# Performance work log

Hardware: AMD Instinct MI355X
Metric: run time of the kernel (lower is better)

Reference implementation:

```python
import jax, jax.numpy as jnp
import numpy as np

B, E, R, A, NV, SEL = 512, 1024, 1024, 512, 196, 36

def _lstm_cell(x, h, c, Wih, bih, Whh, bhh):
    g = x @ Wih.T + bih + h @ Whh.T + bhh
    i, f, gg, o = jnp.split(g, 4, axis=1)  # torch gate order i,f,g,o
    c2 = jax.nn.sigmoid(f) * c + jax.nn.sigmoid(i) * jnp.tanh(gg)
    h2 = jax.nn.sigmoid(o) * jnp.tanh(c2)
    return h2, c2

def _attention(h, feats, p_feats, Wh, bh, Wa, ba):
    # feats: [B,S,R], p_feats: [B,S,A]
    att_h = h @ Wh.T + bh                       # [B,A]
    dot = jnp.tanh(p_feats + att_h[:, None, :])  # [B,S,A]
    scores = jnp.einsum('bsa,a->bs', dot, Wa[0]) + ba[0]
    w = jax.nn.softmax(scores, axis=1)
    return jnp.einsum('bs,bsd->bd', w, feats)

def setup_inputs() -> dict:
    key = jax.random.key(0)
    ks = jax.random.split(key, 32)
    s = 0.02
    inp = {
        'xt': jax.random.normal(ks[0], (B, E), jnp.float32),
        'fc_feats': jax.random.normal(ks[1], (B, R), jnp.float32),
        'att_feats': jax.random.normal(ks[2], (B, NV, R), jnp.float32),
        'p_att_feats': jax.random.normal(ks[3], (B, NV, A), jnp.float32),
        'state_h': jax.random.normal(ks[4], (2, B, R), jnp.float32),
        'state_c': jax.random.normal(ks[5], (2, B, R), jnp.float32),
        # att_lstm: input E + 2R
        'W_ih_att': jax.random.normal(ks[6], (4 * R, E + 2 * R), jnp.float32) * s,
        'b_ih_att': jnp.zeros((4 * R,), jnp.float32),
        'W_hh_att': jax.random.normal(ks[7], (4 * R, R), jnp.float32) * s,
        'b_hh_att': jnp.zeros((4 * R,), jnp.float32),
        # lang_lstm: input 3R
        'W_ih_lang': jax.random.normal(ks[8], (4 * R, 3 * R), jnp.float32) * s,
        'b_ih_lang': jnp.zeros((4 * R,), jnp.float32),
        'W_hh_lang': jax.random.normal(ks[9], (4 * R, R), jnp.float32) * s,
        'b_hh_lang': jnp.zeros((4 * R,), jnp.float32),
        # attention 1
        'Wh2att1': jax.random.normal(ks[10], (A, R), jnp.float32) * s,
        'bh2att1': jnp.zeros((A,), jnp.float32),
        'Walpha1': jax.random.normal(ks[11], (1, A), jnp.float32) * s,
        'balpha1': jnp.zeros((1,), jnp.float32),
        # vf attention
        'Wh2att2': jax.random.normal(ks[12], (A, R), jnp.float32) * s,
        'bh2att2': jnp.zeros((A,), jnp.float32),
        'Walpha2': jax.random.normal(ks[13], (1, A), jnp.float32) * s,
        'balpha2': jnp.zeros((1,), jnp.float32),
        # vf_layer and p_vf
        'W_vf': jax.random.normal(ks[14], (NV, 2 * R), jnp.float32) * s,
        'b_vf': jnp.zeros((NV,), jnp.float32),
        'W_pvf': jax.random.normal(ks[15], (A, R), jnp.float32) * s,
        'b_pvf': jnp.zeros((A,), jnp.float32),
    }
    return inp

def reference(xt, fc_feats, att_feats, p_att_feats, state_h, state_c,
              W_ih_att, b_ih_att, W_hh_att, b_hh_att,
              W_ih_lang, b_ih_lang, W_hh_lang, b_hh_lang,
              Wh2att1, bh2att1, Walpha1, balpha1,
              Wh2att2, bh2att2, Walpha2, balpha2,
              W_vf, b_vf, W_pvf, b_pvf):
    # dropout in eval mode -> identity
    prev_h = state_h[-1]
    att_lstm_input = jnp.concatenate([prev_h, fc_feats, xt], axis=1)
    h_att, c_att = _lstm_cell(att_lstm_input, state_h[0], state_c[0],
                              W_ih_att, b_ih_att, W_hh_att, b_hh_att)
    att = _attention(h_att, att_feats, p_att_feats, Wh2att1, bh2att1, Walpha1, balpha1)
    conc = jnp.concatenate([att, h_att], axis=1)          # [B,2R]
    vf_ha = conc @ W_vf.T + b_vf                          # [B,NV]
    vf_soft = jax.nn.softmax(vf_ha, axis=1)
    _, vf_ix = jax.lax.top_k(vf_soft, SEL)                # [B,SEL] (descending)
    arr1 = jnp.take_along_axis(att_feats, vf_ix[:, :, None], axis=1)  # [B,SEL,R]
    p_vf_feats = arr1 @ W_pvf.T + b_pvf                   # [B,SEL,A]
    vf_att = _attention(h_att, arr1, p_vf_feats, Wh2att2, bh2att2, Walpha2, balpha2)
    lang_lstm_input = jnp.concatenate([vf_att, h_att, att], axis=1)
    h_lang, c_lang = _lstm_cell(lang_lstm_input, state_h[1], state_c[1],
                                W_ih_lang, b_ih_lang, W_hh_lang, b_hh_lang)
    output = h_lang
    new_h = jnp.stack([h_att, h_lang])
    new_c = jnp.stack([c_att, c_lang])
    return output, new_h, new_c
```

## Files before the change

kernel.cpp:

```cpp
#include <hip/hip_runtime.h>

typedef __attribute__((ext_vector_type(4))) float f32x4;
typedef __attribute__((ext_vector_type(8))) _Float16 half8;
typedef __attribute__((ext_vector_type(4))) _Float16 half4;

__device__ __forceinline__ float fast_tanh(float x) {
  float e = __expf(2.f * x);
  return 1.f - 2.f / (e + 1.f);
}
__device__ __forceinline__ float fast_sigmoid(float x) {
  return 1.f / (1.f + __expf(-x));
}

__device__ __forceinline__ void gl_lds16(const _Float16* g, _Float16* l) {
  __builtin_amdgcn_global_load_lds(
      (const __attribute__((address_space(1))) void*)g,
      (__attribute__((address_space(3))) void*)l, 16, 0, 0);
}

template<int SPLIT, int OUT16, int NGUARD, int SWAPXY>
__global__ __launch_bounds__(256) void gemm16(
    const _Float16* __restrict__ Ahp, const _Float16* __restrict__ Alp, int lda,
    const _Float16* __restrict__ Bhp, const _Float16* __restrict__ Blp, int ldb,
    void* __restrict__ Cp, int ldc, long czstride,
    int N, int Kc)
{
  __shared__ _Float16 sAh[2][128 * 32];
  __shared__ _Float16 sBh[2][128 * 32];
  __shared__ _Float16 sAl[SPLIT == 3 ? 2 : 1][SPLIT == 3 ? 128 * 32 : 8];
  __shared__ _Float16 sBl[SPLIT == 3 ? 2 : 1][SPLIT == 3 ? 128 * 32 : 8];

  const int tid = threadIdx.x, lane = tid & 63, wid = tid >> 6;
  const int wm = wid >> 1, wn = wid & 1;
  const int l16 = lane & 15, k8 = lane >> 4;
  const int sr = lane >> 2;
  const int scol = ((lane & 3) ^ ((lane >> 3) & 3)) * 8;
  const int koff = ((k8 ^ ((lane >> 1) & 3))) * 8;

  const int  kt0   = blockIdx.z * Kc;
  const long abase = (long)(SWAPXY ? blockIdx.x : blockIdx.y) * 128;
  const long bbase = (long)(SWAPXY ? blockIdx.y : blockIdx.x) * 128;

  const int r0 = wid * 32 + sr;
  const int r1 = wid * 32 + 16 + sr;
  long br0 = bbase + r0, br1 = bbase + r1;
  if (NGUARD) {
    if (br0 > N - 1) br0 = N - 1;
    if (br1 > N - 1) br1 = N - 1;
  }

  const _Float16* ga0 = Ahp + (abase + r0) * (long)lda + kt0 + scol;
  const _Float16* ga1 = Ahp + (abase + r1) * (long)lda + kt0 + scol;
  const _Float16* gb0 = Bhp + br0 * (long)ldb + kt0 + scol;
  const _Float16* gb1 = Bhp + br1 * (long)ldb + kt0 + scol;
  const _Float16* la0 = SPLIT == 3 ? Alp + (abase + r0) * (long)lda + kt0 + scol : nullptr;
  const _Float16* la1 = SPLIT == 3 ? Alp + (abase + r1) * (long)lda + kt0 + scol : nullptr;
  const _Float16* lb0 = SPLIT == 3 ? Blp + br0 * (long)ldb + kt0 + scol : nullptr;
  const _Float16* lb1 = SPLIT == 3 ? Blp + br1 * (long)ldb + kt0 + scol : nullptr;

  const int e0 = (wid * 32) * 32;
  const int e1 = (wid * 32 + 16) * 32;

  f32x4 acc[4][4];
#pragma unroll
  for (int i = 0; i < 4; i++)
#pragma unroll
    for (int j = 0; j < 4; j++) acc[i][j] = (f32x4){0.f, 0.f, 0.f, 0.f};

  auto STAGE = [&](int buf, int kk) {
    gl_lds16(ga0 + kk, &sAh[buf][e0]);
    gl_lds16(ga1 + kk, &sAh[buf][e1]);
    gl_lds16(gb0 + kk, &sBh[buf][e0]);
    gl_lds16(gb1 + kk, &sBh[buf][e1]);
    if (SPLIT == 3) {
      gl_lds16(la0 + kk, &sAl[buf][e0]);
      gl_lds16(la1 + kk, &sAl[buf][e1]);
      gl_lds16(lb0 + kk, &sBl[buf][e0]);
      gl_lds16(lb1 + kk, &sBl[buf][e1]);
    }
  };

  STAGE(0, 0);

  const int nst = Kc >> 5;
  for (int t = 0; t < nst; t++) {
    const int buf = t & 1;
    if (t + 1 < nst) {
      STAGE(buf ^ 1, (t + 1) * 32);
      if (SPLIT == 3) asm volatile("s_waitcnt vmcnt(8)" ::: "memory");
      else            asm volatile("s_waitcnt vmcnt(4)" ::: "memory");
    } else {
      asm volatile("s_waitcnt vmcnt(0)" ::: "memory");
    }
    __builtin_amdgcn_sched_barrier(0);
    __builtin_amdgcn_s_barrier();
    __builtin_amdgcn_sched_barrier(0);

    half8 ah[4], bh[4];
#pragma unroll
    for (int m = 0; m < 4; m++)
      ah[m] = *(const half8*)&sAh[buf][(wm * 64 + m * 16 + l16) * 32 + koff];
#pragma unroll
    for (int n = 0; n < 4; n++)
      bh[n] = *(const half8*)&sBh[buf][(wn * 64 + n * 16 + l16) * 32 + koff];
#pragma unroll
    for (int m = 0; m < 4; m++)
#pragma unroll
      for (int n = 0; n < 4; n++)
        acc[m][n] = __builtin_amdgcn_mfma_f32_16x16x32_f16(ah[m], bh[n], acc[m][n], 0, 0, 0);
    if (SPLIT == 3) {
      half8 al[4], bl[4];
#pragma unroll
      for (int m = 0; m < 4; m++)
        al[m] = *(const half8*)&sAl[buf][(wm * 64 + m * 16 + l16) * 32 + koff];
#pragma unroll
      for (int n = 0; n < 4; n++)
        bl[n] = *(const half8*)&sBl[buf][(wn * 64 + n * 16 + l16) * 32 + koff];
#pragma unroll
      for (int m = 0; m < 4; m++)
#pragma unroll
        for (int n = 0; n < 4; n++) {
          acc[m][n] = __builtin_amdgcn_mfma_f32_16x16x32_f16(al[m], bh[n], acc[m][n], 0, 0, 0);
          acc[m][n] = __builtin_amdgcn_mfma_f32_16x16x32_f16(ah[m], bl[n], acc[m][n], 0, 0, 0);
        }
    }
    __builtin_amdgcn_sched_barrier(0);
    __builtin_amdgcn_s_barrier();
    __builtin_amdgcn_sched_barrier(0);
  }

  const long czoff = (long)blockIdx.z * czstride;
#pragma unroll
  for (int m = 0; m < 4; m++)
#pragma unroll
    for (int n = 0; n < 4; n++) {
      const long row0 = abase + wm * 64 + m * 16 + (lane >> 4) * 4;
      const long col  = bbase + wn * 64 + n * 16 + l16;
      if (!NGUARD || col < N) {
#pragma unroll
        for (int j = 0; j < 4; j++) {
          const long idx = (row0 + j) * (long)ldc + col + czoff;
          if (OUT16) ((_Float16*)Cp)[idx] = (_Float16)acc[m][n][j];
          else       ((float*)Cp)[idx] = acc[m][n][j];
        }
      }
    }
}

__global__ __launch_bounds__(256) void pack_kernel(
    const float* __restrict__ xt, const float* __restrict__ fc,
    const float* __restrict__ sh,
    _Float16* __restrict__ X1h, _Float16* __restrict__ X1l)
{
  int i = blockIdx.x * 256 + threadIdx.x;
  int b = i >> 10, rr = i & 1023;
  long base = (long)b * 4096;
  float v[4];
  v[0] = sh[524288 + i];
  v[1] = fc[i];
  v[2] = xt[i];
  v[3] = sh[i];
#pragma unroll
  for (int j = 0; j < 4; j++) {
    _Float16 h = (_Float16)v[j];
    X1h[base + j * 1024 + rr] = h;
    X1l[base + j * 1024 + rr] = (_Float16)(v[j] - (float)h);
  }
}

__global__ __launch_bounds__(256) void convertA_kernel(
    const float* __restrict__ WihA, const float* __restrict__ WhhA,
    const float* __restrict__ Wh1, const float* __restrict__ Wh2,
    const float* __restrict__ Wvf, const float* __restrict__ Wpvf,
    _Float16* __restrict__ WcAh, _Float16* __restrict__ WcAl,
    _Float16* __restrict__ W12h, _Float16* __restrict__ Wvfh,
    _Float16* __restrict__ Wvfl, _Float16* __restrict__ Wpvfh)
{
  int bi = blockIdx.x, t = threadIdx.x;
  if (bi < 16384) {
    long e = ((long)bi * 256 + t) * 4;
    int row = (int)(e >> 12), col = (int)(e & 4095);
    const float* src = (col < 3072) ? WihA + (long)row * 3072 + col
                                    : WhhA + (long)row * 1024 + (col - 3072);
    f32x4 v = *(const f32x4*)src;
    half4 h, l;
#pragma unroll
    for (int j = 0; j < 4; j++) { h[j] = (_Float16)v[j]; l[j] = (_Float16)(v[j] - (float)h[j]); }
    *(half4*)&WcAh[e] = h;
    *(half4*)&WcAl[e] = l;
  } else if (bi < 17408) {
    long e = ((long)(bi - 16384) * 256 + t) * 4;
    int row = (int)(e >> 10), col = (int)(e & 1023);
    const float* src = (row < 512) ? Wh1 + (long)row * 1024 + col
                                   : Wh2 + (long)(row - 512) * 1024 + col;
    f32x4 v = *(const f32x4*)src;
    half4 h;
#pragma unroll
    for (int j = 0; j < 4; j++) h[j] = (_Float16)v[j];
    *(half4*)&W12h[e] = h;
  } else if (bi < 17800) {
    long e = ((long)(bi - 17408) * 256 + t) * 4;
    f32x4 v = *(const f32x4*)(Wvf + e);
    half4 h, l;
#pragma unroll
    for (int j = 0; j < 4; j++) { h[j] = (_Float16)v[j]; l[j] = (_Float16)(v[j] - (float)h[j]); }
    *(half4*)&Wvfh[e] = h;
    *(half4*)&Wvfl[e] = l;
  } else {
    long e = ((long)(bi - 17800) * 256 + t) * 4;
    f32x4 v = *(const f32x4*)(Wpvf + e);
    half4 h;
#pragma unroll
    for (int j = 0; j < 4; j++) h[j] = (_Float16)v[j];
    *(half4*)&Wpvfh[e] = h;
  }
}

__global__ __launch_bounds__(256) void convertL_kernel(
    const float* __restrict__ WihL, const float* __restrict__ WhhL,
    _Float16* __restrict__ WcLh)
{
  long e = ((long)blockIdx.x * 256 + threadIdx.x) * 4;
  int row = (int)(e >> 12), col = (int)(e & 4095);
  const float* src = (col < 3072) ? WihL + (long)row * 3072 + col
                                  : WhhL + (long)row * 1024 + (col - 3072);
  f32x4 v = *(const f32x4*)src;
  half4 h;
#pragma unroll
  for (int j = 0; j < 4; j++) h[j] = (_Float16)v[j];
  *(half4*)&WcLh[e] = h;
}

template<int NP, bool H16, bool ATT>
__global__ __launch_bounds__(256) void lstm_act_kernel(
    const void* __restrict__ gp, const float* __restrict__ bih,
    const float* __restrict__ bhh, const float* __restrict__ cin,
    float* __restrict__ hOut, float* __restrict__ cOut,
    _Float16* __restrict__ hatt_h, _Float16* __restrict__ conch,
    _Float16* __restrict__ concl, _Float16* __restrict__ x2h,
    const float* __restrict__ sh, float* __restrict__ hOut2)
{
  const long S = 2097152;
  int i = blockIdx.x * 256 + threadIdx.x;
  int b = i >> 10, rr = i & 1023;
  long gb = (long)b * 4096;
  float g4[4];
#pragma unroll
  for (int q = 0; q < 4; q++) {
    float s = 0.f;
#pragma unroll
    for (int z = 0; z < NP; z++) {
      long off = (long)z * S + gb + q * 1024 + rr;
      s += H16 ? (float)((const _Float16*)gp)[off] : ((const float*)gp)[off];
    }
    g4[q] = s + bih[q * 1024 + rr] + bhh[q * 1024 + rr];
  }
  float c  = cin[i];
  float c2 = fast_sigmoid(g4[1]) * c + fast_sigmoid(g4[0]) * fast_tanh(g4[2]);
  float h2 = fast_sigmoid(g4[3]) * fast_tanh(c2);
  hOut[i] = h2;
  cOut[i] = c2;
  if (hOut2) hOut2[i] = h2;
  if (ATT) {
    _Float16 hh = (_Float16)h2;
    hatt_h[i] = hh;
    conch[(long)b * 2048 + 1024 + rr] = hh;
    concl[(long)b * 2048 + 1024 + rr] = (_Float16)(h2 - (float)hh);
    x2h[(long)b * 4096 + 1024 + rr] = hh;
    x2h[(long)b * 4096 + 3072 + rr] = (_Float16)sh[524288 + i];
  }
}

__global__ __launch_bounds__(256) void reduce_atth_kernel(
    const float* __restrict__ p, float* __restrict__ o)
{
  int i = (blockIdx.x * 256 + threadIdx.x) * 4;
  f32x4 a = *(const f32x4*)(p + i);
  f32x4 b = *(const f32x4*)(p + 524288 + i);
  f32x4 c = *(const f32x4*)(p + 1048576 + i);
  f32x4 d = *(const f32x4*)(p + 1572864 + i);
  *(f32x4*)(o + i) = a + b + c + d;
}

__global__ __launch_bounds__(256) void score1_kernel(
    const float* __restrict__ pf, const float* __restrict__ atth,
    const float* __restrict__ bh,
    const float* __restrict__ walpha, const float* __restrict__ balpha,
    float* __restrict__ out, int nrows)
{
  int gw = blockIdx.x * 4 + (threadIdx.x >> 6);
  int lane = threadIdx.x & 63;
  if (gw >= nrows) return;
  int b = gw / 196;
  const float* p  = pf + (long)gw * 512 + lane * 8;
  const float* ah = atth + (long)b * 1024 + lane * 8;
  const float* bp = bh + lane * 8;
  const float* wp = walpha + lane * 8;
  float acc = 0.f;
#pragma unroll
  for (int u = 0; u < 2; u++) {
    f32x4 pv = *(const f32x4*)(p + u * 4);
    f32x4 av = *(const f32x4*)(ah + u * 4);
    f32x4 bv = *(const f32x4*)(bp + u * 4);
    f32x4 wv = *(const f32x4*)(wp + u * 4);
#pragma unroll
    for (int j = 0; j < 4; j++)
      acc += fast_tanh(pv[j] + av[j] + bv[j]) * wv[j];
  }
#pragma unroll
  for (int off = 32; off; off >>= 1) acc += __shfl_xor(acc, off);
  if (lane == 0) out[gw] = acc + balpha[0];
}

__global__ __launch_bounds__(256) void attsum1_kernel(
    const float* __restrict__ scores, const float* __restrict__ feats,
    _Float16* __restrict__ conch, _Float16* __restrict__ concl, _Float16* __restrict__ x2h)
{
  __shared__ float w[256];
  int b = blockIdx.x, t = threadIdx.x;
  float s0 = (t < 196) ? scores[b * 196 + t] : -3.0e38f;
  w[t] = s0;
  __syncthreads();
  float mx = -3.0e38f;
  for (int i = 0; i < 196; i++) mx = fmaxf(mx, w[i]);
  float sum = 0.f;
  for (int i = 0; i < 196; i++) sum += __expf(w[i] - mx);
  float inv = 1.f / sum;
  __syncthreads();
  if (t < 196) w[t] = __expf(s0 - mx) * inv;
  __syncthreads();
  f32x4 acc = (f32x4){0.f, 0.f, 0.f, 0.f};
  const float* fb = feats + (long)b * 200704 + t * 4;
  for (int s0i = 0; s0i < 192; s0i += 8) {
    f32x4 v[8];
#pragma unroll
    for (int u = 0; u < 8; u++) v[u] = *(const f32x4*)(fb + (long)(s0i + u) * 1024);
#pragma unroll
    for (int u = 0; u < 8; u++) {
      float ws = w[s0i + u];
#pragma unroll
      for (int j = 0; j < 4; j++) acc[j] += ws * v[u][j];
    }
  }
#pragma unroll
  for (int u = 192; u < 196; u++) {
    float ws = w[u];
    f32x4 v = *(const f32x4*)(fb + (long)u * 1024);
#pragma unroll
    for (int j = 0; j < 4; j++) acc[j] += ws * v[j];
  }
  half4 h, l;
#pragma unroll
  for (int j = 0; j < 4; j++) { h[j] = (_Float16)acc[j]; l[j] = (_Float16)(acc[j] - (float)h[j]); }
  *(half4*)&conch[(long)b * 2048 + t * 4] = h;
  *(half4*)&concl[(long)b * 2048 + t * 4] = l;
  *(half4*)&x2h[(long)b * 4096 + 2048 + t * 4] = h;
}

__global__ __launch_bounds__(256) void vfatt_kernel(
    const _Float16* __restrict__ pvf16, const float* __restrict__ atth2,
    const float* __restrict__ bh2att2, const float* __restrict__ b_pvf,
    const float* __restrict__ walpha2, const float* __restrict__ balpha2,
    const _Float16* __restrict__ arr1h, _Float16* __restrict__ x2h)
{
  __shared__ float w[40];
  int b = blockIdx.x, tid = threadIdx.x;
  int lane = tid & 63, wv = tid >> 6;

  float add[8], wal[8];
#pragma unroll
  for (int u = 0; u < 8; u++) {
    int a = lane * 8 + u;
    add[u] = atth2[(long)b * 1024 + a] + bh2att2[a] + b_pvf[a];
    wal[u] = walpha2[a];
  }
  for (int j = wv; j < 36; j += 4) {
    half8 hv = *(const half8*)&pvf16[((long)b * 36 + j) * 512 + lane * 8];
    float acc = 0.f;
#pragma unroll
    for (int u = 0; u < 8; u++)
      acc += fast_tanh((float)hv[u] + add[u]) * wal[u];
#pragma unroll
    for (int off = 32; off; off >>= 1) acc += __shfl_xor(acc, off);
    if (lane == 0) w[j] = acc + balpha2[0];
  }
  __syncthreads();
  float mx = -3.0e38f;
  for (int i = 0; i < 36; i++) mx = fmaxf(mx, w[i]);
  float sum = 0.f;
  for (int i = 0; i < 36; i++) sum += __expf(w[i] - mx);
  float inv = 1.f / sum;
  __syncthreads();
  if (tid < 36) w[tid] = __expf(w[tid] - mx) * inv;
  __syncthreads();
  f32x4 acc = (f32x4){0.f, 0.f, 0.f, 0.f};
  const _Float16* fb = arr1h + (long)b * 36 * 1024 + tid * 4;
#pragma unroll 4
  for (int s = 0; s < 36; s++) {
    float ws = w[s];
    half4 v = *(const half4*)(fb + (long)s * 1024);
#pragma unroll
    for (int j = 0; j < 4; j++) acc[j] += ws * (float)v[j];
  }
  half4 h;
#pragma unroll
  for (int j = 0; j < 4; j++) h[j] = (_Float16)acc[j];
  *(half4*)&x2h[(long)b * 4096 + tid * 4] = h;
}

template<int NP>
__global__ __launch_bounds__(64) void topk_kernel(
    const float* __restrict__ vfp, const float* __restrict__ b_vf, int* __restrict__ ix)
{
  int b = blockIdx.x;
  int lane = threadIdx.x;
  float v[4];
#pragma unroll
  for (int j = 0; j < 4; j++) {
    int s = lane + 64 * j;
    float sum = -3.0e38f;
    if (s < 196) {
      sum = b_vf[s];
#pragma unroll
      for (int z = 0; z < NP; z++) sum += vfp[(long)z * 100352 + b * 196 + s];
    }
    v[j] = sum;
  }
  for (int it = 0; it < 36; it++) {
    float bv = -3.0e38f; int bs = 1 << 20;
#pragma unroll
    for (int j = 0; j < 4; j++) {
      int s = lane + 64 * j;
      if (v[j] > bv) { bv = v[j]; bs = s; }
    }
#pragma unroll
    for (int off = 32; off; off >>= 1) {
      float ov = __shfl_xor(bv, off);
      int   os = __shfl_xor(bs, off);
      if (ov > bv || (ov == bv && os < bs)) { bv = ov; bs = os; }
    }
    if ((bs & 63) == lane) v[bs >> 6] = -3.0e38f;
    if (lane == 0) ix[b * 36 + it] = bs;
  }
}

__global__ __launch_bounds__(256) void gather_conv_kernel(
    const float* __restrict__ feats, const int* __restrict__ ix, _Float16* __restrict__ dst)
{
  int bj = blockIdx.x;
  int b = bj / 36;
  int s = ix[bj];
  int t = threadIdx.x;
  f32x4 v = *(const f32x4*)(feats + ((long)b * 196 + s) * 1024 + t * 4);
  half4 h;
#pragma unroll
  for (int j = 0; j < 4; j++) h[j] = (_Float16)v[j];
  *(half4*)&dst[(long)bj * 1024 + t * 4] = h;
}

extern "C" void kernel_launch(void* const* d_in, const int* in_sizes, int n_in,
                              void* d_out, int out_size, void* d_ws, size_t ws_size,
                              hipStream_t stream) {
  const float* xt        = (const float*)d_in[0];
  const float* fc_feats  = (const float*)d_in[1];
  const float* att_feats = (const float*)d_in[2];
  const float* p_att     = (const float*)d_in[3];
  const float* state_h   = (const float*)d_in[4];
  const float* state_c   = (const float*)d_in[5];
  const float* b_ih_att  = (const float*)d_in[7];
  const float* b_hh_att  = (const float*)d_in[9];
  const float* b_ih_lang = (const float*)d_in[11];
  const float* b_hh_lang = (const float*)d_in[13];
  const float* bh2att1   = (const float*)d_in[15];
  const float* Walpha1   = (const float*)d_in[16];
  const float* balpha1   = (const float*)d_in[17];
  const float* bh2att2   = (const float*)d_in[19];
  const float* Walpha2   = (const float*)d_in[20];
  const float* balpha2   = (const float*)d_in[21];
  const float* b_vf      = (const float*)d_in[23];
  const float* b_pvf     = (const float*)d_in[25];

  float* out = (float*)d_out;
  float* W = (float*)d_ws;

  _Float16* WcAh   = (_Float16*)(W + 0);
  _Float16* WcAl   = (_Float16*)(W + 8388608);
  _Float16* WcLh   = (_Float16*)(W + 16777216);
  _Float16* X1h    = (_Float16*)(W + 25165824);
  _Float16* X1l    = (_Float16*)(W + 26214400);
  float*    g1p    = W + 27262976;
  _Float16* hatt_h = (_Float16*)(W + 35651584);
  _Float16* W12h   = (_Float16*)(W + 35913728);
  _Float16* Wvfh   = (_Float16*)(W + 36438016);
  _Float16* Wvfl   = (_Float16*)(W + 36638720);
  _Float16* Wpvfh  = (_Float16*)(W + 36839424);
  float*    atthp  = W + 37101568;
  float*    atth   = W + 39198720;
  _Float16* conch  = (_Float16*)(W + 39723008);
  _Float16* concl  = (_Float16*)(W + 40247296);
  _Float16* X2h    = (_Float16*)(W + 40771584);
  float*    scores1= W + 41820160;
  float*    vfhap  = W + 41920512;
  int*      vfix   = (int*)(W + 43526144);
  _Float16* arr1h  = (_Float16*)(W + 43544576);
  _Float16* pvf16  = (_Float16*)(W + 52981760);
  _Float16* g2ph   = (_Float16*)(W + 57700352);

  float* out_h0 = out + 524288;
  float* out_h1 = out + 2 * 524288;
  float* out_c0 = out + 3 * 524288;
  float* out_c1 = out + 4 * 524288;

  pack_kernel<<<2048, 256, 0, stream>>>(xt, fc_feats, state_h, X1h, X1l);

  convertA_kernel<<<18312, 256, 0, stream>>>(
      (const float*)d_in[6], (const float*)d_in[8],
      (const float*)d_in[14], (const float*)d_in[18],
      (const float*)d_in[22], (const float*)d_in[24],
      WcAh, WcAl, W12h, Wvfh, Wvfl, Wpvfh);

  gemm16<3, 0, 0, 0><<<dim3(32, 4, 4), 256, 0, stream>>>(
      X1h, X1l, 4096, WcAh, WcAl, 4096, g1p, 4096, 2097152, 4096, 1024);

  convertL_kernel<<<16384, 256, 0, stream>>>(
      (const float*)d_in[10], (const float*)d_in[12], WcLh);

  lstm_act_kernel<4, false, true><<<2048, 256, 0, stream>>>(
      g1p, b_ih_att, b_hh_att, state_c, out_h0, out_c0,
      hatt_h, conch, concl, X2h, state_h, nullptr);

  gemm16<1, 0, 0, 0><<<dim3(8, 4, 4), 256, 0, stream>>>(
      hatt_h, nullptr, 1024, W12h, nullptr, 1024, atthp, 1024, 524288, 1024, 256);
  reduce_atth_kernel<<<512, 256, 0, stream>>>(atthp, atth);

  score1_kernel<<<25088, 256, 0, stream>>>(
      p_att, atth, bh2att1, Walpha1, balpha1, scores1, 100352);

  attsum1_kernel<<<512, 256, 0, stream>>>(scores1, att_feats, conch, concl, X2h);

  gemm16<3, 0, 1, 0><<<dim3(2, 4, 16), 256, 0, stream>>>(
      conch, concl, 2048, Wvfh, Wvfl, 2048, vfhap, 196, 100352, 196, 128);

  topk_kernel<16><<<512, 64, 0, stream>>>(vfhap, b_vf, vfix);

  gather_conv_kernel<<<18432, 256, 0, stream>>>(att_feats, vfix, arr1h);

  gemm16<1, 1, 0, 1><<<dim3(144, 4, 1), 256, 0, stream>>>(
      arr1h, nullptr, 1024, Wpvfh, nullptr, 1024, pvf16, 512, 0, 512, 1024);

  vfatt_kernel<<<512, 256, 0, stream>>>(
      pvf16, atth + 512, bh2att2, b_pvf, Walpha2, balpha2, arr1h, X2h);

  gemm16<1, 1, 0, 0><<<dim3(32, 4, 4), 256, 0, stream>>>(
      X2h, nullptr, 4096, WcLh, nullptr, 4096, g2ph, 4096, 2097152, 4096, 1024);

  lstm_act_kernel<4, true, false><<<2048, 256, 0, stream>>>(
      g2ph, b_ih_lang, b_hh_lang, state_c + 524288, out, out_c1,
      nullptr, nullptr, nullptr, nullptr, nullptr, out_h1);
}
```

Before: 411.9 us.

## Unify split-fp16 GEMM into concatenated K segments with 4-stage pipelined LDS buffers

Replaces the split-precision GEMM path (three MFMAs per k-step over hi/lo A and B tiles) with a single-MFMA kernel over an extended K dimension. The activations are laid out as [hi | lo | hi] and the weights are selected per segment as hi/hi/lo, so the K loop covers three times the length. The LDS pipeline goes from double buffering to a 4-deep ring with three stages in flight, and the trailing barrier is removed. All weight conversion and input packing kernels are merged into one prep launch, which removes launches and makes the code more regular, at the cost of a larger packed activation buffer and more loop iterations.

```diff
diff --git a/kernel.cpp b/kernel.cpp
--- a/kernel.cpp
+++ b/kernel.cpp
@@ -18,17 +18,15 @@
       (__attribute__((address_space(3))) void*)l, 16, 0, 0);
 }
 
-template<int SPLIT, int OUT16, int NGUARD, int SWAPXY>
+template<int SEGLOG, int OUT16, int NGUARD, int SWAPXY>
 __global__ __launch_bounds__(256) void gemm16(
-    const _Float16* __restrict__ Ahp, const _Float16* __restrict__ Alp, int lda,
+    const _Float16* __restrict__ Ahp, int lda,
     const _Float16* __restrict__ Bhp, const _Float16* __restrict__ Blp, int ldb,
     void* __restrict__ Cp, int ldc, long czstride,
     int N, int Kc)
 {
-  __shared__ _Float16 sAh[2][128 * 32];
-  __shared__ _Float16 sBh[2][128 * 32];
-  __shared__ _Float16 sAl[SPLIT == 3 ? 2 : 1][SPLIT == 3 ? 128 * 32 : 8];
-  __shared__ _Float16 sBl[SPLIT == 3 ? 2 : 1][SPLIT == 3 ? 128 * 32 : 8];
+  __shared__ _Float16 sA[4][128 * 32];
+  __shared__ _Float16 sB[4][128 * 32];
 
   const int tid = threadIdx.x, lane = tid & 63, wid = tid >> 6;
   const int wm = wid >> 1, wn = wid & 1;
@@ -49,14 +47,10 @@
     if (br1 > N - 1) br1 = N - 1;
   }
 
-  const _Float16* ga0 = Ahp + (abase + r0) * (long)lda + kt0 + scol;
-  const _Float16* ga1 = Ahp + (abase + r1) * (long)lda + kt0 + scol;
-  const _Float16* gb0 = Bhp + br0 * (long)ldb + kt0 + scol;
-  const _Float16* gb1 = Bhp + br1 * (long)ldb + kt0 + scol;
-  const _Float16* la0 = SPLIT == 3 ? Alp + (abase + r0) * (long)lda + kt0 + scol : nullptr;
-  const _Float16* la1 = SPLIT == 3 ? Alp + (abase + r1) * (long)lda + kt0 + scol : nullptr;
-  const _Float16* lb0 = SPLIT == 3 ? Blp + br0 * (long)ldb + kt0 + scol : nullptr;
-  const _Float16* lb1 = SPLIT == 3 ? Blp + br1 * (long)ldb + kt0 + scol : nullptr;
+  const _Float16* ga0 = Ahp + (abase + r0) * (long)lda + scol;
+  const _Float16* ga1 = Ahp + (abase + r1) * (long)lda + scol;
+  const long bro0 = br0 * (long)ldb + scol;
+  const long bro1 = br1 * (long)ldb + scol;
 
   const int e0 = (wid * 32) * 32;
   const int e1 = (wid * 32 + 16) * 32;
@@ -67,66 +61,51 @@
 #pragma unroll
     for (int j = 0; j < 4; j++) acc[i][j] = (f32x4){0.f, 0.f, 0.f, 0.f};
 
-  auto STAGE = [&](int buf, int kk) {
-    gl_lds16(ga0 + kk, &sAh[buf][e0]);
-    gl_lds16(ga1 + kk, &sAh[buf][e1]);
-    gl_lds16(gb0 + kk, &sBh[buf][e0]);
-    gl_lds16(gb1 + kk, &sBh[buf][e1]);
-    if (SPLIT == 3) {
-      gl_lds16(la0 + kk, &sAl[buf][e0]);
-      gl_lds16(la1 + kk, &sAl[buf][e1]);
-      gl_lds16(lb0 + kk, &sBl[buf][e0]);
-      gl_lds16(lb1 + kk, &sBl[buf][e1]);
-    }
+  auto STAGE = [&](int buf, int kt) {
+    gl_lds16(ga0 + kt, &sA[buf][e0]);
+    gl_lds16(ga1 + kt, &sA[buf][e1]);
+    const _Float16* bp;
+    int kloc;
+    if (SEGLOG) {
+      int seg = kt >> SEGLOG;
+      kloc = kt & ((1 << SEGLOG) - 1);
+      bp = (seg < 2) ? Bhp : Blp;
+    } else {
+      bp = Bhp; kloc = kt;
+    }
+    gl_lds16(bp + bro0 + kloc, &sB[buf][e0]);
+    gl_lds16(bp + bro1 + kloc, &sB[buf][e1]);
   };
 
-  STAGE(0, 0);
-
   const int nst = Kc >> 5;
+  STAGE(0, kt0);
+  if (nst > 1) STAGE(1, kt0 + 32);
+  if (nst > 2) STAGE(2, kt0 + 64);
+
   for (int t = 0; t < nst; t++) {
-    const int buf = t & 1;
-    if (t + 1 < nst) {
-      STAGE(buf ^ 1, (t + 1) * 32);
-      if (SPLIT == 3) asm volatile("s_waitcnt vmcnt(8)" ::: "memory");
-      else            asm volatile("s_waitcnt vmcnt(4)" ::: "memory");
-    } else {
-      asm volatile("s_waitcnt vmcnt(0)" ::: "memory");
-    }
+    const int buf = t & 3;
+    const int rem = nst - 1 - t;
+    if (rem >= 2)      asm volatile("s_waitcnt vmcnt(8)" ::: "memory");
+    else if (rem == 1) asm volatile("s_waitcnt vmcnt(4)" ::: "memory");
+    else               asm volatile("s_waitcnt vmcnt(0)" ::: "memory");
     __builtin_amdgcn_sched_barrier(0);
     __builtin_amdgcn_s_barrier();
     __builtin_amdgcn_sched_barrier(0);
 
+    if (t + 3 < nst) STAGE((t + 3) & 3, kt0 + (t + 3) * 32);
+
     half8 ah[4], bh[4];
 #pragma unroll
     for (int m = 0; m < 4; m++)
-      ah[m] = *(const half8*)&sAh[buf][(wm * 64 + m * 16 + l16) * 32 + koff];
+      ah[m] = *(const half8*)&sA[buf][(wm * 64 + m * 16 + l16) * 32 + koff];
 #pragma unroll
     for (int n = 0; n < 4; n++)
-      bh[n] = *(const half8*)&sBh[buf][(wn * 64 + n * 16 + l16) * 32 + koff];
+      bh[n] = *(const half8*)&sB[buf][(wn * 64 + n * 16 + l16) * 32 + koff];
 #pragma unroll
     for (int m = 0; m < 4; m++)
 #pragma unroll
       for (int n = 0; n < 4; n++)
         acc[m][n] = __builtin_amdgcn_mfma_f32_16x16x32_f16(ah[m], bh[n], acc[m][n], 0, 0, 0);
-    if (SPLIT == 3) {
-      half8 al[4], bl[4];
-#pragma unroll
-      for (int m = 0; m < 4; m++)
-        al[m] = *(const half8*)&sAl[buf][(wm * 64 + m * 16 + l16) * 32 + koff];
-#pragma unroll
-      for (int n = 0; n < 4; n++)
-        bl[n] = *(const half8*)&sBl[buf][(wn * 64 + n * 16 + l16) * 32 + koff];
-#pragma unroll
-      for (int m = 0; m < 4; m++)
-#pragma unroll
-        for (int n = 0; n < 4; n++) {
-          acc[m][n] = __builtin_amdgcn_mfma_f32_16x16x32_f16(al[m], bh[n], acc[m][n], 0, 0, 0);
-          acc[m][n] = __builtin_amdgcn_mfma_f32_16x16x32_f16(ah[m], bl[n], acc[m][n], 0, 0, 0);
-        }
-    }
-    __builtin_amdgcn_sched_barrier(0);
-    __builtin_amdgcn_s_barrier();
-    __builtin_amdgcn_sched_barrier(0);
   }
 
   const long czoff = (long)blockIdx.z * czstride;
@@ -147,34 +126,17 @@
     }
 }
 
-__global__ __launch_bounds__(256) void pack_kernel(
+__global__ __launch_bounds__(256) void prep_kernel(
+    const float* __restrict__ WihA, const float* __restrict__ WhhA,
+    const float* __restrict__ WihL, const float* __restrict__ WhhL,
+    const float* __restrict__ Wh1, const float* __restrict__ Wh2,
+    const float* __restrict__ Wvf, const float* __restrict__ Wpvf,
     const float* __restrict__ xt, const float* __restrict__ fc,
     const float* __restrict__ sh,
-    _Float16* __restrict__ X1h, _Float16* __restrict__ X1l)
-{
-  int i = blockIdx.x * 256 + threadIdx.x;
-  int b = i >> 10, rr = i & 1023;
-  long base = (long)b * 4096;
-  float v[4];
-  v[0] = sh[524288 + i];
-  v[1] = fc[i];
-  v[2] = xt[i];
-  v[3] = sh[i];
-#pragma unroll
-  for (int j = 0; j < 4; j++) {
-    _Float16 h = (_Float16)v[j];
-    X1h[base + j * 1024 + rr] = h;
-    X1l[base + j * 1024 + rr] = (_Float16)(v[j] - (float)h);
-  }
-}
-
-__global__ __launch_bounds__(256) void convertA_kernel(
-    const float* __restrict__ WihA, const float* __restrict__ WhhA,
-    const float* __restrict__ Wh1, const float* __restrict__ Wh2,
-    const float* __restrict__ Wvf, const float* __restrict__ Wpvf,
     _Float16* __restrict__ WcAh, _Float16* __restrict__ WcAl,
-    _Float16* __restrict__ W12h, _Float16* __restrict__ Wvfh,
-    _Float16* __restrict__ Wvfl, _Float16* __restrict__ Wpvfh)
+    _Float16* __restrict__ WcLh, _Float16* __restrict__ W12h,
+    _Float16* __restrict__ Wvfh, _Float16* __restrict__ Wvfl,
+    _Float16* __restrict__ Wpvfh, _Float16* __restrict__ X1p)
 {
   int bi = blockIdx.x, t = threadIdx.x;
   if (bi < 16384) {
@@ -188,8 +150,18 @@
     for (int j = 0; j < 4; j++) { h[j] = (_Float16)v[j]; l[j] = (_Float16)(v[j] - (float)h[j]); }
     *(half4*)&WcAh[e] = h;
     *(half4*)&WcAl[e] = l;
-  } else if (bi < 17408) {
+  } else if (bi < 32768) {
     long e = ((long)(bi - 16384) * 256 + t) * 4;
+    int row = (int)(e >> 12), col = (int)(e & 4095);
+    const float* src = (col < 3072) ? WihL + (long)row * 3072 + col
+                                    : WhhL + (long)row * 1024 + (col - 3072);
+    f32x4 v = *(const f32x4*)src;
+    half4 h;
+#pragma unroll
+    for (int j = 0; j < 4; j++) h[j] = (_Float16)v[j];
+    *(half4*)&WcLh[e] = h;
+  } else if (bi < 33792) {
+    long e = ((long)(bi - 32768) * 256 + t) * 4;
     int row = (int)(e >> 10), col = (int)(e & 1023);
     const float* src = (row < 512) ? Wh1 + (long)row * 1024 + col
                                    : Wh2 + (long)(row - 512) * 1024 + col;
@@ -198,37 +170,38 @@
 #pragma unroll
     for (int j = 0; j < 4; j++) h[j] = (_Float16)v[j];
     *(half4*)&W12h[e] = h;
-  } else if (bi < 17800) {
-    long e = ((long)(bi - 17408) * 256 + t) * 4;
+  } else if (bi < 34184) {
+    long e = ((long)(bi - 33792) * 256 + t) * 4;
     f32x4 v = *(const f32x4*)(Wvf + e);
     half4 h, l;
 #pragma unroll
     for (int j = 0; j < 4; j++) { h[j] = (_Float16)v[j]; l[j] = (_Float16)(v[j] - (float)h[j]); }
     *(half4*)&Wvfh[e] = h;
     *(half4*)&Wvfl[e] = l;
-  } else {
-    long e = ((long)(bi - 17800) * 256 + t) * 4;
+  } else if (bi < 34696) {
+    long e = ((long)(bi - 34184) * 256 + t) * 4;
     f32x4 v = *(const f32x4*)(Wpvf + e);
     half4 h;
 #pragma unroll
     for (int j = 0; j < 4; j++) h[j] = (_Float16)v[j];
     *(half4*)&Wpvfh[e] = h;
-  }
-}
-
-__global__ __launch_bounds__(256) void convertL_kernel(
-    const float* __restrict__ WihL, const float* __restrict__ WhhL,
-    _Float16* __restrict__ WcLh)
-{
-  long e = ((long)blockIdx.x * 256 + threadIdx.x) * 4;
-  int row = (int)(e >> 12), col = (int)(e & 4095);
-  const float* src = (col < 3072) ? WihL + (long)row * 3072 + col
-                                  : WhhL + (long)row * 1024 + (col - 3072);
-  f32x4 v = *(const f32x4*)src;
-  half4 h;
-#pragma unroll
-  for (int j = 0; j < 4; j++) h[j] = (_Float16)v[j];
-  *(half4*)&WcLh[e] = h;
+  } else {
+    int i = (bi - 34696) * 256 + t;
+    int b = i >> 10, rr = i & 1023;
+    long base = (long)b * 12288;
+    float v[4];
+    v[0] = sh[524288 + i];
+    v[1] = fc[i];
+    v[2] = xt[i];
+    v[3] = sh[i];
+#pragma unroll
+    for (int j = 0; j < 4; j++) {
+      _Float16 h = (_Float16)v[j];
+      X1p[base + j * 1024 + rr] = h;
+      X1p[base + 4096 + j * 1024 + rr] = (_Float16)(v[j] - (float)h);
+      X1p[base + 8192 + j * 1024 + rr] = h;
+    }
+  }
 }
 
 template<int NP, bool H16, bool ATT>
@@ -236,9 +209,9 @@
     const void* __restrict__ gp, const float* __restrict__ bih,
     const float* __restrict__ bhh, const float* __restrict__ cin,
     float* __restrict__ hOut, float* __restrict__ cOut,
-    _Float16* __restrict__ hatt_h, _Float16* __restrict__ conch,
-    _Float16* __restrict__ concl, _Float16* __restrict__ x2h,
-    const float* __restrict__ sh, float* __restrict__ hOut2)
+    _Float16* __restrict__ hatt_h, _Float16* __restrict__ concp,
+    _Float16* __restrict__ x2h, const float* __restrict__ sh,
+    float* __restrict__ hOut2)
 {
   const long S = 2097152;
   int i = blockIdx.x * 256 + threadIdx.x;
@@ -264,8 +237,10 @@
   if (ATT) {
     _Float16 hh = (_Float16)h2;
     hatt_h[i] = hh;
-    conch[(long)b * 2048 + 1024 + rr] = hh;
-    concl[(long)b * 2048 + 1024 + rr] = (_Float16)(h2 - (float)hh);
+    long cb = (long)b * 6144 + 1024 + rr;
+    concp[cb] = hh;
+    concp[cb + 2048] = (_Float16)(h2 - (float)hh);
+    concp[cb + 4096] = hh;
     x2h[(long)b * 4096 + 1024 + rr] = hh;
     x2h[(long)b * 4096 + 3072 + rr] = (_Float16)sh[524288 + i];
   }
@@ -314,7 +289,7 @@
 
 __global__ __launch_bounds__(256) void attsum1_kernel(
     const float* __restrict__ scores, const float* __restrict__ feats,
-    _Float16* __restrict__ conch, _Float16* __restrict__ concl, _Float16* __restrict__ x2h)
+    _Float16* __restrict__ concp, _Float16* __restrict__ x2h)
 {
   __shared__ float w[256];
   int b = blockIdx.x, t = threadIdx.x;
@@ -352,8 +327,10 @@
   half4 h, l;
 #pragma unroll
   for (int j = 0; j < 4; j++) { h[j] = (_Float16)acc[j]; l[j] = (_Float16)(acc[j] - (float)h[j]); }
-  *(half4*)&conch[(long)b * 2048 + t * 4] = h;
-  *(half4*)&concl[(long)b * 2048 + t * 4] = l;
+  long cb = (long)b * 6144 + t * 4;
+  *(half4*)&concp[cb] = h;
+  *(half4*)&concp[cb + 2048] = l;
+  *(half4*)&concp[cb + 4096] = h;
   *(half4*)&x2h[(long)b * 4096 + 2048 + t * 4] = h;
 }
 
@@ -486,75 +463,70 @@
   _Float16* WcAh   = (_Float16*)(W + 0);
   _Float16* WcAl   = (_Float16*)(W + 8388608);
   _Float16* WcLh   = (_Float16*)(W + 16777216);
-  _Float16* X1h    = (_Float16*)(W + 25165824);
-  _Float16* X1l    = (_Float16*)(W + 26214400);
-  float*    g1p    = W + 27262976;
-  _Float16* hatt_h = (_Float16*)(W + 35651584);
-  _Float16* W12h   = (_Float16*)(W + 35913728);
-  _Float16* Wvfh   = (_Float16*)(W + 36438016);
-  _Float16* Wvfl   = (_Float16*)(W + 36638720);
-  _Float16* Wpvfh  = (_Float16*)(W + 36839424);
-  float*    atthp  = W + 37101568;
-  float*    atth   = W + 39198720;
-  _Float16* conch  = (_Float16*)(W + 39723008);
-  _Float16* concl  = (_Float16*)(W + 40247296);
-  _Float16* X2h    = (_Float16*)(W + 40771584);
-  float*    scores1= W + 41820160;
-  float*    vfhap  = W + 41920512;
-  int*      vfix   = (int*)(W + 43526144);
-  _Float16* arr1h  = (_Float16*)(W + 43544576);
-  _Float16* pvf16  = (_Float16*)(W + 52981760);
-  _Float16* g2ph   = (_Float16*)(W + 57700352);
+  _Float16* X1p    = (_Float16*)(W + 25165824);
+  float*    g1p    = W + 28311552;
+  _Float16* hatt_h = (_Float16*)(W + 36700160);
+  _Float16* W12h   = (_Float16*)(W + 36962304);
+  _Float16* Wvfh   = (_Float16*)(W + 37486592);
+  _Float16* Wvfl   = (_Float16*)(W + 37687296);
+  _Float16* Wpvfh  = (_Float16*)(W + 37888000);
+  float*    atthp  = W + 38150144;
+  float*    atth   = W + 40247296;
+  _Float16* concp  = (_Float16*)(W + 40771584);
+  _Float16* X2h    = (_Float16*)(W + 42344448);
+  float*    scores1= W + 43393024;
+  float*    vfhap  = W + 43493376;
+  int*      vfix   = (int*)(W + 45099008);
+  _Float16* arr1h  = (_Float16*)(W + 45117440);
+  _Float16* pvf16  = (_Float16*)(W + 54554624);
+  _Float16* g2ph   = (_Float16*)(W + 59273216);
 
   float* out_h0 = out + 524288;
   float* out_h1 = out + 2 * 524288;
   float* out_c0 = out + 3 * 524288;
   float* out_c1 = out + 4 * 524288;
 
-  pack_kernel<<<2048, 256, 0, stream>>>(xt, fc_feats, state_h, X1h, X1l);
-
-  convertA_kernel<<<18312, 256, 0, stream>>>(
+  prep_kernel<<<36744, 256, 0, stream>>>(
       (const float*)d_in[6], (const float*)d_in[8],
+      (const float*)d_in[10], (const float*)d_in[12],
       (const float*)d_in[14], (const float*)d_in[18],
       (const float*)d_in[22], (const float*)d_in[24],
-      WcAh, WcAl, W12h, Wvfh, Wvfl, Wpvfh);
-
-  gemm16<3, 0, 0, 0><<<dim3(32, 4, 4), 256, 0, stream>>>(
-      X1h, X1l, 4096, WcAh, WcAl, 4096, g1p, 4096, 2097152, 4096, 1024);
-
-  convertL_kernel<<<16384, 256, 0, stream>>>(
-      (const float*)d_in[10], (const float*)d_in[12], WcLh);
+      xt, fc_feats, state_h,
+      WcAh, WcAl, WcLh, W12h, Wvfh, Wvfl, Wpvfh, X1p);
+
+  gemm16<12, 0, 0, 0><<<dim3(32, 4, 4), 256, 0, stream>>>(
+      X1p, 12288, WcAh, WcAl, 4096, g1p, 4096, 2097152, 4096, 3072);
 
   lstm_act_kernel<4, false, true><<<2048, 256, 0, stream>>>(
       g1p, b_ih_att, b_hh_att, state_c, out_h0, out_c0,
-      hatt_h, conch, concl, X2h, state_h, nullptr);
-
-  gemm16<1, 0, 0, 0><<<dim3(8, 4, 4), 256, 0, stream>>>(
-      hatt_h, nullptr, 1024, W12h, nullptr, 1024, atthp, 1024, 524288, 1024, 256);
+      hatt_h, concp, X2h, state_h, nullptr);
+
+  gemm16<0, 0, 0, 0><<<dim3(8, 4, 4), 256, 0, stream>>>(
+      hatt_h, 1024, W12h, nullptr, 1024, atthp, 1024, 524288, 1024, 256);
   reduce_atth_kernel<<<512, 256, 0, stream>>>(atthp, atth);
 
   score1_kernel<<<25088, 256, 0, stream>>>(
       p_att, atth, bh2att1, Walpha1, balpha1, scores1, 100352);
 
-  attsum1_kernel<<<512, 256, 0, stream>>>(scores1, att_feats, conch, concl, X2h);
-
-  gemm16<3, 0, 1, 0><<<dim3(2, 4, 16), 256, 0, stream>>>(
-      conch, concl, 2048, Wvfh, Wvfl, 2048, vfhap, 196, 100352, 196, 128);
+  attsum1_kernel<<<512, 256, 0, stream>>>(scores1, att_feats, concp, X2h);
+
+  gemm16<11, 0, 1, 0><<<dim3(2, 4, 16), 256, 0, stream>>>(
+      concp, 6144, Wvfh, Wvfl, 2048, vfhap, 196, 100352, 196, 384);
 
   topk_kernel<16><<<512, 64, 0, stream>>>(vfhap, b_vf, vfix);
 
   gather_conv_kernel<<<18432, 256, 0, stream>>>(att_feats, vfix, arr1h);
 
-  gemm16<1, 1, 0, 1><<<dim3(144, 4, 1), 256, 0, stream>>>(
-      arr1h, nullptr, 1024, Wpvfh, nullptr, 1024, pvf16, 512, 0, 512, 1024);
+  gemm16<0, 1, 0, 1><<<dim3(144, 4, 1), 256, 0, stream>>>(
+      arr1h, 1024, Wpvfh, nullptr, 1024, pvf16, 512, 0, 512, 1024);
 
   vfatt_kernel<<<512, 256, 0, stream>>>(
       pvf16, atth + 512, bh2att2, b_pvf, Walpha2, balpha2, arr1h, X2h);
 
-  gemm16<1, 1, 0, 0><<<dim3(32, 4, 4), 256, 0, stream>>>(
-      X2h, nullptr, 4096, WcLh, nullptr, 4096, g2ph, 4096, 2097152, 4096, 1024);
+  gemm16<0, 1, 0, 0><<<dim3(32, 4, 4), 256, 0, stream>>>(
+      X2h, 4096, WcLh, nullptr, 4096, g2ph, 4096, 2097152, 4096, 1024);
 
   lstm_act_kernel<4, true, false><<<2048, 256, 0, stream>>>(
       g2ph, b_ih_lang, b_hh_lang, state_c + 524288, out, out_c1,
-      nullptr, nullptr, nullptr, nullptr, nullptr, out_h1);
-}
+      nullptr, nullptr, nullptr, nullptr, out_h1);
+}
```

Measured after the change: 452.4 us. 1.1x slower.
